# Performance work log

Hardware: AMD Instinct MI355X
Metric: run time of the kernel (lower is better)

Reference implementation:

```python
import jax, jax.numpy as jnp
import numpy as np

B, CTX_DIM, CTX_SIZE, HID, SEQLEN = 32, 1024, 2048, 1024, 64


def setup_inputs() -> dict:
    key = jax.random.key(0)
    k1, k2, k3, k4 = jax.random.split(key, 4)
    hidden = jax.random.normal(k1, (1, B, HID), dtype=jnp.float32)
    contextvects = jax.random.normal(k2, (B, CTX_DIM, CTX_SIZE), dtype=jnp.float32)
    # nn.Linear(context_dim, hidden_size): W is [hidden_size, context_dim]
    W = jax.random.normal(k3, (HID, CTX_DIM), dtype=jnp.float32) / np.sqrt(CTX_DIM)
    b = jax.random.normal(k4, (HID,), dtype=jnp.float32) * 0.01
    return {"seqlen": SEQLEN, "hidden": hidden, "contextvects": contextvects, "W": W, "b": b}


def reference(seqlen, hidden, contextvects, W, b):
    # Original torch loop recomputes the identical quantities every timestep;
    # compute once and broadcast across seqlen (same math, no redundancy).
    # contextvects: [B, D, C]; project each context position: [B, C, H]
    context_proj = jnp.einsum('bdc,hd->bch', contextvects, W) + b
    # hidden: [1, B, H] -> scores [B, C]
    scores = jnp.einsum('bch,bh->bc', context_proj, hidden[0])
    attn_weights = jax.nn.softmax(scores, axis=1)  # softmax over context positions
    ctx = jnp.einsum('bdc,bc->bd', contextvects, attn_weights)  # [B, D]
    return jnp.broadcast_to(ctx[None, :, :], (seqlen, ctx.shape[0], ctx.shape[1]))
```

## Files before the change

kernel.cpp:

```cpp
#include <hip/hip_runtime.h>
#include <math.h>

#define NB 32
#define ND 1024
#define NC 2048
#define NH 1024
#define NSEQ 64
#define CCHUNK 32
#define NCHUNK (NC / CCHUNK)

#define GLD_TO_LDS(g, l)                                                     \
  __builtin_amdgcn_global_load_lds(                                          \
      (const __attribute__((address_space(1))) void*)(g),                    \
      (__attribute__((address_space(3))) void*)(l), 16, 0, 0)

__global__ __launch_bounds__(128) void k1_v(const float* __restrict__ hidden,
                                            const float* __restrict__ W,
                                            float* __restrict__ v) {
  const int b = blockIdx.x >> 3;
  const int d = ((blockIdx.x & 7) << 7) + threadIdx.x;
  const float* hb = hidden + b * NH;
  float acc = 0.f;
#pragma unroll 16
  for (int h = 0; h < NH; ++h) acc += hb[h] * W[h * ND + d];
  v[b * ND + d] = acc;
}

__global__ __launch_bounds__(512) void k2_main(const float* __restrict__ ctx,
                                               const float* __restrict__ v,
                                               float* __restrict__ accp,
                                               float* __restrict__ ml) {
  __shared__ __align__(16) float tile[ND * CCHUNK];
  __shared__ __align__(16) float sred[64 * 32];
  __shared__ __align__(16) float pf[CCHUNK];

  const int t = threadIdx.x;
  const int bid = blockIdx.x;
  const int b = bid >> 6;
  const int c0 = (bid & (NCHUNK - 1)) << 5;
  const int dp = t >> 3;
  const int cg = t & 7;
  const int w = __builtin_amdgcn_readfirstlane(t >> 6);

  const float* gbase = ctx + (size_t)b * ND * NC + (size_t)dp * NC + c0 + cg * 4;
#pragma unroll
  for (int j = 0; j < 16; ++j) {
    GLD_TO_LDS(gbase + (size_t)(64 * NC) * j, tile + 2048 * j + (w << 8));
  }

  float vsr[16];
#pragma unroll
  for (int j = 0; j < 16; ++j) vsr[j] = v[b * ND + dp + 64 * j];

  __syncthreads();

  float4 s4 = make_float4(0.f, 0.f, 0.f, 0.f);
  const float* myw = tile + 4 * t;
#pragma unroll
  for (int j = 0; j < 16; ++j) {
    float4 x = *(const float4*)(myw + 2048 * j);
    float vd = vsr[j];
    s4.x += x.x * vd; s4.y += x.y * vd; s4.z += x.z * vd; s4.w += x.w * vd;
  }
  *(float4*)(sred + 4 * t) = s4;
  __syncthreads();

  if (t < 32) {
    float s = 0.f;
#pragma unroll
    for (int q = 0; q < 64; ++q) s += sred[32 * q + t];
    float mm = s;
#pragma unroll
    for (int off = 16; off; off >>= 1) mm = fmaxf(mm, __shfl_xor(mm, off, 32));
    float e = __expf(s - mm);
    float l = e;
#pragma unroll
    for (int off = 16; off; off >>= 1) l += __shfl_xor(l, off, 32);
    pf[t] = e;
    if (t == 0) { ml[bid * 2] = mm; ml[bid * 2 + 1] = l; }
  }
  __syncthreads();

  float4 pr[8];
#pragma unroll
  for (int j = 0; j < 8; ++j)
    pr[j] = *(const float4*)(pf + (((j + t) & 7) << 2));

  float* ao = accp + (size_t)bid * ND;
#pragma unroll
  for (int k = 0; k < 2; ++k) {
    const int d = t + 512 * k;
    const float* tr = tile + d * CCHUNK;
    float a = 0.f;
#pragma unroll
    for (int j = 0; j < 8; ++j) {
      const int jr = (j + t) & 7;
      float4 x = *(const float4*)(tr + jr * 4);
      float4 pp = pr[j];
      a += x.x * pp.x + x.y * pp.y + x.z * pp.z + x.w * pp.w;
    }
    ao[d] = a;
  }
}

__global__ __launch_bounds__(128) void k3_combine_bcast(
    const float* __restrict__ accp, const float* __restrict__ ml,
    float* __restrict__ out) {
  __shared__ float sc[NCHUNK];
  __shared__ float sinv_s;
  const int b = blockIdx.x >> 3;
  const int dslice = blockIdx.x & 7;
  const int t = threadIdx.x;

  if (t < NCHUNK) {
    float mi = ml[(b * NCHUNK + t) * 2];
    float li = ml[(b * NCHUNK + t) * 2 + 1];
    float mg = mi;
#pragma unroll
    for (int off = 32; off; off >>= 1) mg = fmaxf(mg, __shfl_xor(mg, off, 64));
    float scale = __expf(mi - mg);
    float dpart = scale * li;
#pragma unroll
    for (int off = 32; off; off >>= 1) dpart += __shfl_xor(dpart, off, 64);
    sc[t] = scale;
    if (t == 0) sinv_s = 1.0f / dpart;
  }
  __syncthreads();
  const float sinv = sinv_s;

  const int d = dslice * 128 + t;
  const float* ap = accp + (size_t)b * NCHUNK * ND + d;
  float acc = 0.f;
#pragma unroll 16
  for (int i = 0; i < NCHUNK; ++i) acc += sc[i] * ap[(size_t)i * ND];
  acc *= sinv;

  float* op = out + b * ND + d;
#pragma unroll 8
  for (int s = 0; s < NSEQ; ++s) op[(size_t)s * NB * ND] = acc;
}

extern "C" void kernel_launch(void* const* d_in, const int* in_sizes, int n_in,
                              void* d_out, int out_size, void* d_ws, size_t ws_size,
                              hipStream_t stream) {
  (void)in_sizes; (void)n_in; (void)out_size; (void)ws_size;
  const float* hidden = (const float*)d_in[1];
  const float* ctxv   = (const float*)d_in[2];
  const float* W      = (const float*)d_in[3];
  float* out = (float*)d_out;

  char* ws = (char*)d_ws;
  float* v    = (float*)(ws);
  float* ml   = (float*)(ws + 131072);
  float* accp = (float*)(ws + 131072 + 16384);

  k1_v<<<256, 128, 0, stream>>>(hidden, W, v);
  k2_main<<<NB * NCHUNK, 512, 0, stream>>>(ctxv, v, accp, ml);
  k3_combine_bcast<<<256, 128, 0, stream>>>(accp, ml, out);
}
```

Baseline: 422.9 us.

## Keep context tile in registers instead of LDS and split k1 reduction

The main kernel no longer stages the 128KB context tile in LDS through global_load_lds. Each thread keeps its 16 float4 values in registers and reuses them for both the score and the weighted-sum passes, reducing across lanes with shuffles. This frees LDS so more blocks can be resident (launch bounds request 4 per CU), at the cost of higher register pressure. Separately, k1 splits the hidden-dimension reduction across two thread halves and combines them through shared memory, giving it more parallelism.

```diff
diff --git a/kernel.cpp b/kernel.cpp
--- a/kernel.cpp
+++ b/kernel.cpp
@@ -9,30 +9,30 @@
 #define CCHUNK 32
 #define NCHUNK (NC / CCHUNK)
 
-#define GLD_TO_LDS(g, l)                                                     \
-  __builtin_amdgcn_global_load_lds(                                          \
-      (const __attribute__((address_space(1))) void*)(g),                    \
-      (__attribute__((address_space(3))) void*)(l), 16, 0, 0)
-
-__global__ __launch_bounds__(128) void k1_v(const float* __restrict__ hidden,
+__global__ __launch_bounds__(256) void k1_v(const float* __restrict__ hidden,
                                             const float* __restrict__ W,
                                             float* __restrict__ v) {
+  __shared__ float part[128];
   const int b = blockIdx.x >> 3;
-  const int d = ((blockIdx.x & 7) << 7) + threadIdx.x;
-  const float* hb = hidden + b * NH;
+  const int dl = threadIdx.x & 127;
+  const int d = ((blockIdx.x & 7) << 7) + dl;
+  const int hh = threadIdx.x >> 7;
+  const float* hb = hidden + b * NH + hh * 512;
+  const float* Wp = W + (size_t)hh * 512 * ND + d;
   float acc = 0.f;
 #pragma unroll 16
-  for (int h = 0; h < NH; ++h) acc += hb[h] * W[h * ND + d];
-  v[b * ND + d] = acc;
+  for (int h = 0; h < 512; ++h) acc += hb[h] * Wp[(size_t)h * ND];
+  if (hh) part[dl] = acc;
+  __syncthreads();
+  if (!hh) v[b * ND + d] = acc + part[dl];
 }
 
-__global__ __launch_bounds__(512) void k2_main(const float* __restrict__ ctx,
-                                               const float* __restrict__ v,
-                                               float* __restrict__ accp,
-                                               float* __restrict__ ml) {
-  __shared__ __align__(16) float tile[ND * CCHUNK];
+__global__ __launch_bounds__(512, 4) void k2_main(const float* __restrict__ ctx,
+                                                  const float* __restrict__ v,
+                                                  float* __restrict__ accp,
+                                                  float* __restrict__ ml) {
   __shared__ __align__(16) float sred[64 * 32];
-  __shared__ __align__(16) float pf[CCHUNK];
+  __shared__ float pf[CCHUNK];
 
   const int t = threadIdx.x;
   const int bid = blockIdx.x;
@@ -40,27 +40,23 @@
   const int c0 = (bid & (NCHUNK - 1)) << 5;
   const int dp = t >> 3;
   const int cg = t & 7;
-  const int w = __builtin_amdgcn_readfirstlane(t >> 6);
 
-  const float* gbase = ctx + (size_t)b * ND * NC + (size_t)dp * NC + c0 + cg * 4;
+  const float* g = ctx + (size_t)b * ND * NC + (size_t)dp * NC + c0 + (cg << 2);
+  float4 x[16];
+#pragma unroll
+  for (int j = 0; j < 16; ++j) x[j] = *(const float4*)(g + (size_t)j * (64 * NC));
+
+  float vsr[16];
+  const float* vb = v + b * ND + dp;
+#pragma unroll
+  for (int j = 0; j < 16; ++j) vsr[j] = vb[j * 64];
+
+  float4 s4 = make_float4(0.f, 0.f, 0.f, 0.f);
 #pragma unroll
   for (int j = 0; j < 16; ++j) {
-    GLD_TO_LDS(gbase + (size_t)(64 * NC) * j, tile + 2048 * j + (w << 8));
-  }
-
-  float vsr[16];
-#pragma unroll
-  for (int j = 0; j < 16; ++j) vsr[j] = v[b * ND + dp + 64 * j];
-
-  __syncthreads();
-
-  float4 s4 = make_float4(0.f, 0.f, 0.f, 0.f);
-  const float* myw = tile + 4 * t;
-#pragma unroll
-  for (int j = 0; j < 16; ++j) {
-    float4 x = *(const float4*)(myw + 2048 * j);
-    float vd = vsr[j];
-    s4.x += x.x * vd; s4.y += x.y * vd; s4.z += x.z * vd; s4.w += x.w * vd;
+    const float vd = vsr[j];
+    s4.x += x[j].x * vd; s4.y += x[j].y * vd;
+    s4.z += x[j].z * vd; s4.w += x[j].w * vd;
   }
   *(float4*)(sred + 4 * t) = s4;
   __syncthreads();
@@ -81,25 +77,15 @@
   }
   __syncthreads();
 
-  float4 pr[8];
-#pragma unroll
-  for (int j = 0; j < 8; ++j)
-    pr[j] = *(const float4*)(pf + (((j + t) & 7) << 2));
-
+  const float4 p4 = *(const float4*)(pf + (cg << 2));
   float* ao = accp + (size_t)bid * ND;
 #pragma unroll
-  for (int k = 0; k < 2; ++k) {
-    const int d = t + 512 * k;
-    const float* tr = tile + d * CCHUNK;
-    float a = 0.f;
-#pragma unroll
-    for (int j = 0; j < 8; ++j) {
-      const int jr = (j + t) & 7;
-      float4 x = *(const float4*)(tr + jr * 4);
-      float4 pp = pr[j];
-      a += x.x * pp.x + x.y * pp.y + x.z * pp.z + x.w * pp.w;
-    }
-    ao[d] = a;
+  for (int j = 0; j < 16; ++j) {
+    float aj = x[j].x * p4.x + x[j].y * p4.y + x[j].z * p4.z + x[j].w * p4.w;
+    aj += __shfl_xor(aj, 1, 64);
+    aj += __shfl_xor(aj, 2, 64);
+    aj += __shfl_xor(aj, 4, 64);
+    if (cg == (j & 7)) ao[dp + (j << 6)] = aj;
   }
 }
 
@@ -154,7 +140,7 @@
   float* ml   = (float*)(ws + 131072);
   float* accp = (float*)(ws + 131072 + 16384);
 
-  k1_v<<<256, 128, 0, stream>>>(hidden, W, v);
+  k1_v<<<256, 256, 0, stream>>>(hidden, W, v);
   k2_main<<<NB * NCHUNK, 512, 0, stream>>>(ctxv, v, accp, ml);
   k3_combine_bcast<<<256, 128, 0, stream>>>(accp, ml, out);
 }
```

Result: faster. 403.8 us (-4.5%).
